# Optimization experiments

Measured on AMD Instinct MI355X. Metric: run time of the kernel, lower is better.

Reference implementation:

```python
import jax, jax.numpy as jnp
import numpy as np

DIM = 512
HEADS = 8
DIM_HEAD = 64  # default dim_head used for scale, matches DIM//HEADS here
SCALE = DIM_HEAD ** -0.5
B, X, Y = 8, 32, 32


def setup_inputs() -> dict:
    key = jax.random.key(0)
    k0, k1, k2, k3 = jax.random.split(key, 4)
    fmap = jax.random.normal(k0, (B, DIM, X, Y), dtype=jnp.float32)
    # 1x1 convs as matrices: weight [out, in]
    Wqkvl = jax.random.normal(k1, (4 * DIM, DIM), dtype=jnp.float32) * (DIM ** -0.5)
    Wout = jax.random.normal(k2, (DIM, DIM), dtype=jnp.float32) * (DIM ** -0.5)
    bout = jax.random.normal(k3, (DIM,), dtype=jnp.float32) * 0.01
    return {"fmap": fmap, "Wqkvl": Wqkvl, "Wout": Wout, "bout": bout}


def reference(fmap, Wqkvl, Wout, bout):
    b, c, x, y = fmap.shape
    h, d = HEADS, c // HEADS
    n = x * y
    # 1x1 conv projection to q,k,v,L
    qkvL = jnp.einsum('oc,bcxy->boxy', Wqkvl, fmap)  # [b, 4c, x, y]
    q, k, v, L = jnp.split(qkvL, 4, axis=1)
    # 'b (h d) x y -> b h (x y) d'
    def to_tokens(t):
        return t.reshape(b, h, d, n).transpose(0, 1, 3, 2)
    q, k, v, L = map(to_tokens, (q, k, v, L))
    dots = jnp.einsum('bhid,bhjd->bhij', q, k) * SCALE  # [b,h,n,n]
    attn = jax.nn.softmax(dots, axis=-1)
    out = jnp.einsum('bhij,bhjd->bhid', attn, v) + L  # [b,h,n,d]
    # 'b h (x y) d -> b (h d) x y'
    out = out.transpose(0, 1, 3, 2).reshape(b, c, x, y)
    # output 1x1 conv with bias (dropout=0 -> identity)
    out = jnp.einsum('oc,bcxy->boxy', Wout, out) + bout[None, :, None, None]
    return out
```

## Files before the change

### kernel.cpp

```cpp
#include <hip/hip_runtime.h>

#define Bn 8
#define Cn 512
#define Hn 8
#define Dn 64
#define Nn 1024
#define SCALEQ 0.18033688011112042f

typedef unsigned short u16;
typedef unsigned short u16x8 __attribute__((ext_vector_type(8)));
typedef unsigned short u16x4 __attribute__((ext_vector_type(4)));
typedef short s16x4 __attribute__((ext_vector_type(4)));
typedef float f32x4 __attribute__((ext_vector_type(4)));
typedef __bf16 bf16x8 __attribute__((ext_vector_type(8)));

__device__ __forceinline__ u16 f2bf(float f){
  unsigned u = __float_as_uint(f);
  u += 0x7fffu + ((u >> 16) & 1u);
  return (u16)(u >> 16);
}
__device__ __forceinline__ float bf2f(u16 h){
  return __uint_as_float(((unsigned)h) << 16);
}
__device__ __forceinline__ f32x4 mfma16(u16x8 a, u16x8 b, f32x4 c){
  return __builtin_amdgcn_mfma_f32_16x16x32_bf16(
      __builtin_bit_cast(bf16x8, a), __builtin_bit_cast(bf16x8, b), c, 0, 0, 0);
}
__device__ __forceinline__ f32x4 mfma16k16(u16x4 a, u16x4 b, f32x4 c){
  return __builtin_amdgcn_mfma_f32_16x16x16bf16_1k(
      __builtin_bit_cast(s16x4, a), __builtin_bit_cast(s16x4, b), c, 0, 0, 0);
}

__device__ __forceinline__ void gload16(const u16* src, u16* dst){
  __builtin_amdgcn_global_load_lds(
      (const __attribute__((address_space(1))) unsigned int*)src,
      (__attribute__((address_space(3))) unsigned int*)dst, 16, 0, 0);
}

__global__ __launch_bounds__(256) void k_convert2(const float* __restrict__ s1,
                                                  const float* __restrict__ s2,
                                                  u16* __restrict__ d1, u16* __restrict__ d2,
                                                  int n1, int n2){
  int i = blockIdx.x * 256 + threadIdx.x;
  const float* s; u16* d; int j;
  if (i < n1){ s = s1; d = d1; j = i; }
  else { if (i >= n1 + n2) return; s = s2; d = d2; j = i - n1; }
  float4 f = reinterpret_cast<const float4*>(s)[j];
  u16x4 o;
  o[0] = f2bf(f.x); o[1] = f2bf(f.y); o[2] = f2bf(f.z); o[3] = f2bf(f.w);
  reinterpret_cast<u16x4*>(d)[j] = o;
}

__global__ __launch_bounds__(256) void k_transpose(const float* __restrict__ fmap,
                                                   u16* __restrict__ fmapT){
  __shared__ float tile[64][33];
  const int n0 = blockIdx.x * 32, c0 = blockIdx.y * 64, b = blockIdx.z;
  const int tx = threadIdx.x & 31, ty = threadIdx.x >> 5;
  const float* src = fmap + ((size_t)b * Cn + c0) * Nn + n0;
#pragma unroll
  for (int i = 0; i < 8; i++) tile[ty + 8*i][tx] = src[(size_t)(ty + 8*i) * Nn + tx];
  __syncthreads();
  const int nr = threadIdx.x >> 3;
  const int cj = (threadIdx.x & 7) * 8;
  u16x8 o;
#pragma unroll
  for (int k = 0; k < 8; k++) o[k] = f2bf(tile[cj + k][nr]);
  *reinterpret_cast<u16x8*>(fmapT + ((size_t)b * Nn + n0 + nr) * Cn + c0 + cj) = o;
}

__device__ __forceinline__ void stage64(const u16* g, size_t ldg, u16* lbase, int w, int lane){
#pragma unroll
  for (int s = 0; s < 2; s++){
    int row = s*32 + w*8 + (lane>>3);
    gload16(g + (size_t)row*ldg + (((lane&7) ^ (row&7)) * 8), lbase + (s*32 + w*8)*64);
  }
}
__device__ __forceinline__ void stage128x32(const u16* g, size_t ldg, u16* lbase, int w, int lane){
#pragma unroll
  for (int s = 0; s < 2; s++){
    int row = s*64 + w*16 + (lane>>2);
    gload16(g + (size_t)row*ldg + (((lane&3) ^ (row&3)) * 8), lbase + (s*64 + w*16)*32);
  }
}
__device__ __forceinline__ void stage64x32(const u16* g, size_t ldg, u16* lbase, int w, int lane){
  int row = w*16 + (lane>>2);
  gload16(g + (size_t)row*ldg + (((lane&3) ^ (row&3)) * 8), lbase + (w*16)*32);
}

__device__ __forceinline__ void gemm_fma(const u16x8 (&af)[4], const u16x8 (&bf)[4],
                                         f32x4 (&acc)[4][4]){
#pragma unroll
  for (int i = 0; i < 4; i++)
#pragma unroll
    for (int j = 0; j < 4; j++)
      acc[i][j] = mfma16(af[i], bf[j], acc[i][j]);
}

__device__ __forceinline__ void gemm_nt_128(const u16* __restrict__ Ap, int lda,
                                            const u16* __restrict__ Bp, int ldb,
                                            u16* sA, u16* sB,
                                            f32x4 (&acc)[4][4]){
  const int tid = threadIdx.x;
  const int w = tid >> 6, lane = tid & 63, r = lane & 15, g = lane >> 4;
  const int wi = w >> 1, wj = w & 1;
  stage128x32(Ap, lda, sA, w, lane);
  stage128x32(Bp, ldb, sB, w, lane);
  for (int ks = 0; ks < Cn/32; ks++){
    __syncthreads();
    const int cur = ks & 1;
    if (ks + 1 < Cn/32){
      stage128x32(Ap + (ks+1)*32, lda, sA + (cur^1)*128*32, w, lane);
      stage128x32(Bp + (ks+1)*32, ldb, sB + (cur^1)*128*32, w, lane);
    }
    const u16* Al = sA + cur*128*32;
    const u16* Bl = sB + cur*128*32;
    u16x8 af[4], bf[4];
#pragma unroll
    for (int t = 0; t < 4; t++){
      int ar = wi*64 + t*16 + r;
      af[t] = *reinterpret_cast<const u16x8*>(&Al[ar*32 + ((g ^ (ar&3)) * 8)]);
      int br = wj*64 + t*16 + r;
      bf[t] = *reinterpret_cast<const u16x8*>(&Bl[br*32 + ((g ^ (br&3)) * 8)]);
    }
    gemm_fma(af, bf, acc);
  }
}

__global__ __launch_bounds__(256) void k_gemm1(const u16* __restrict__ fmapT,
                                               const u16* __restrict__ W1,
                                               u16* __restrict__ Qb, u16* __restrict__ Kb,
                                               u16* __restrict__ Vt, u16* __restrict__ Lb){
  __shared__ u16 sA[2*128*32], sB[2*128*32];
  const int lin = blockIdx.x;
  const int wid = (lin & 7) * 128 + (lin >> 3);
  const int ob = wid & 15, nb = (wid >> 4) & 7, b = wid >> 7;
  const int w = threadIdx.x >> 6, wi = w >> 1, wj = w & 1;
  const int lane = threadIdx.x & 63, r = lane & 15, g = lane >> 4;
  const int seg = ob >> 2;

  f32x4 acc[4][4];
  const f32x4 z = {0.f, 0.f, 0.f, 0.f};
#pragma unroll
  for (int i = 0; i < 4; i++)
#pragma unroll
    for (int j = 0; j < 4; j++) acc[i][j] = z;

  const u16* fbase = fmapT + (size_t)b * Nn * Cn;

  if (seg != 2){
    gemm_nt_128(fbase + (size_t)(nb*128) * Cn, Cn, W1 + (size_t)(ob*128) * Cn, Cn, sA, sB, acc);
    u16* dst = (seg == 0) ? Qb : (seg == 1 ? Kb : Lb);
    const float sc = (seg == 0) ? SCALEQ : 1.0f;
#pragma unroll
    for (int it = 0; it < 4; it++)
#pragma unroll
      for (int jt = 0; jt < 4; jt++)
#pragma unroll
        for (int rr = 0; rr < 4; rr++){
          int n = nb*128 + wi*64 + it*16 + 4*g + rr;
          int o = ob*128 + wj*64 + jt*16 + r;
          dst[((size_t)b * Nn + n) * Cn + (o & 511)] = f2bf(acc[it][jt][rr] * sc);
        }
  } else {
    gemm_nt_128(W1 + (size_t)(ob*128) * Cn, Cn, fbase + (size_t)(nb*128) * Cn, Cn, sA, sB, acc);
#pragma unroll
    for (int it = 0; it < 4; it++)
#pragma unroll
      for (int jt = 0; jt < 4; jt++)
#pragma unroll
        for (int rr = 0; rr < 4; rr++){
          int o = ob*128 + wi*64 + it*16 + 4*g + rr;
          int oo = o - 1024;
          int h = oo >> 6, d = oo & 63;
          int n = nb*128 + wj*64 + jt*16 + r;
          Vt[(((size_t)b * Hn + h) * Dn + d) * Nn + n] = f2bf(acc[it][jt][rr]);
        }
  }
}

__device__ __forceinline__ void attn_tile(const u16* Kc, const u16* Vc,
                                          const u16* kbase, const u16* vbase, int next,
                                          u16* Kn, u16* Vn,
                                          int w, int lane, int r, int g,
                                          u16x8 qA0, u16x8 qA1, u16x8 qB0, u16x8 qB1,
                                          f32x4 (&accA)[4], f32x4 (&accB)[4],
                                          f32x4& accSA, f32x4& accSB){
  const f32x4 z = {0.f, 0.f, 0.f, 0.f};
  __syncthreads();
  if (next < 16){
    stage64(kbase + (size_t)next*64*Cn, Cn, Kn, w, lane);
    stage64(vbase + next*64,            Nn, Vn, w, lane);
  }
  f32x4 sA[4], sB[4];
#pragma unroll
  for (int t = 0; t < 4; t++){
    int row = 16*t + r;
    u16x8 k0 = *reinterpret_cast<const u16x8*>(&Kc[row*64 + ((g     ^ (r&7)) * 8)]);
    u16x8 k1 = *reinterpret_cast<const u16x8*>(&Kc[row*64 + (((4+g) ^ (r&7)) * 8)]);
    sA[t] = mfma16(k0, qA0, z); sA[t] = mfma16(k1, qA1, sA[t]);
    sB[t] = mfma16(k0, qB0, z); sB[t] = mfma16(k1, qB1, sB[t]);
  }
  u16x4 pA[4], pB[4];
#pragma unroll
  for (int t = 0; t < 4; t++)
#pragma unroll
    for (int j = 0; j < 4; j++){
      pA[t][j] = __builtin_bit_cast(u16, (__bf16)exp2f(sA[t][j]));
      pB[t][j] = __builtin_bit_cast(u16, (__bf16)exp2f(sB[t][j]));
    }
  const u16x4 ones = {0x3F80u, 0x3F80u, 0x3F80u, 0x3F80u};
#pragma unroll
  for (int t = 0; t < 4; t++){
    accSA = mfma16k16(ones, pA[t], accSA);
    accSB = mfma16k16(ones, pB[t], accSB);
  }
#pragma unroll
  for (int s = 0; s < 4; s++)
#pragma unroll
    for (int dt = 0; dt < 4; dt++){
      int row = dt*16 + r;
      u16x4 vf = *reinterpret_cast<const u16x4*>(
          &Vc[row*64 + (((2*s + (g>>1)) ^ (r&7)) * 8) + (g&1)*4]);
      accA[dt] = mfma16k16(vf, pA[s], accA[dt]);
      accB[dt] = mfma16k16(vf, pB[s], accB[dt]);
    }
}

__global__ __launch_bounds__(256, 4) void k_attn(const u16* __restrict__ Qb,
                                                 const u16* __restrict__ Kb,
                                                 const u16* __restrict__ Vt,
                                                 const u16* __restrict__ Lb,
                                                 u16* __restrict__ tok){
  __shared__ u16 Kl[2*64*64], Vl[2*64*64];
  const int bid = blockIdx.x;
  const int w0 = (bid & 7) * 64 + (bid >> 3);
  const int qblk = w0 & 7, h = (w0 >> 3) & 7, b = w0 >> 6;
  const int w = threadIdx.x >> 6, lane = threadIdx.x & 63;
  const int r = lane & 15, g = lane >> 4;
  const int qA = qblk * 128 + w * 16;
  const int qB = qA + 64;

  const u16* qrowA = Qb + ((size_t)b * Nn + qA + r) * Cn + h * Dn + 8 * g;
  const u16* qrowB = Qb + ((size_t)b * Nn + qB + r) * Cn + h * Dn + 8 * g;
  u16x8 qA0 = *reinterpret_cast<const u16x8*>(qrowA);
  u16x8 qA1 = *reinterpret_cast<const u16x8*>(qrowA + 32);
  u16x8 qB0 = *reinterpret_cast<const u16x8*>(qrowB);
  u16x8 qB1 = *reinterpret_cast<const u16x8*>(qrowB + 32);

  const u16* kbase = Kb + (size_t)b * Nn * Cn + h * Dn;
  const u16* vbase = Vt + ((size_t)b * Hn + h) * Dn * Nn;

  f32x4 accA[4], accB[4];
  const f32x4 z = {0.f, 0.f, 0.f, 0.f};
#pragma unroll
  for (int dt = 0; dt < 4; dt++){ accA[dt] = z; accB[dt] = z; }
  f32x4 accSA = z, accSB = z;

  u16* Kl0 = Kl, *Kl1 = Kl + 64*64;
  u16* Vl0 = Vl, *Vl1 = Vl + 64*64;
  stage64(kbase, Cn, Kl0, w, lane);
  stage64(vbase, Nn, Vl0, w, lane);

  for (int tile = 0; tile < 16; tile += 2){
    attn_tile(Kl0, Vl0, kbase, vbase, tile + 1, Kl1, Vl1, w, lane, r, g,
              qA0, qA1, qB0, qB1, accA, accB, accSA, accSB);
    attn_tile(Kl1, Vl1, kbase, vbase, tile + 2, Kl0, Vl0, w, lane, r, g,
              qA0, qA1, qB0, qB1, accA, accB, accSA, accSB);
  }

  float linvA = 1.0f / accSA[0];
  float linvB = 1.0f / accSB[0];
#pragma unroll
  for (int half = 0; half < 2; half++){
    const int n = (half ? qB : qA) + r;
    const float linv = half ? linvB : linvA;
    const f32x4* acc = half ? accB : accA;
    const u16* lrow = Lb + ((size_t)b * Nn + n) * Cn + h * Dn;
    u16* trow = tok + ((size_t)b * Nn + n) * Cn + h * Dn;
#pragma unroll
    for (int dt = 0; dt < 4; dt++){
      u16x4 lv = *reinterpret_cast<const u16x4*>(lrow + dt*16 + 4*g);
      u16x4 ov;
#pragma unroll
      for (int rr = 0; rr < 4; rr++)
        ov[rr] = f2bf(acc[dt][rr] * linv + bf2f(lv[rr]));
      *reinterpret_cast<u16x4*>(trow + dt*16 + 4*g) = ov;
    }
  }
}

__global__ __launch_bounds__(256) void k_gemm2(const u16* __restrict__ tok,
                                               const u16* __restrict__ Wo,
                                               const float* __restrict__ bout,
                                               float* __restrict__ out){
  __shared__ u16 sA[2*64*32], sB[2*128*32];
  const int lin = blockIdx.x;
  const int wid = (lin & 7) * 64 + (lin >> 3);
  const int ob = wid & 7, nb = (wid >> 3) & 7, b = wid >> 6;
  const int w = threadIdx.x >> 6, wi = w >> 1, wj = w & 1;
  const int lane = threadIdx.x & 63, r = lane & 15, g = lane >> 4;

  f32x4 acc[2][4];
  const f32x4 z = {0.f, 0.f, 0.f, 0.f};
#pragma unroll
  for (int i = 0; i < 2; i++)
#pragma unroll
    for (int j = 0; j < 4; j++) acc[i][j] = z;

  const u16* Ap = Wo + (size_t)(ob*64) * Cn;
  const u16* Bp = tok + (size_t)b * Nn * Cn + (size_t)(nb*128) * Cn;

  stage64x32(Ap, Cn, sA, w, lane);
  stage128x32(Bp, Cn, sB, w, lane);
  for (int ks = 0; ks < Cn/32; ks++){
    __syncthreads();
    const int cur = ks & 1;
    if (ks + 1 < Cn/32){
      stage64x32(Ap + (ks+1)*32, Cn, sA + (cur^1)*64*32, w, lane);
      stage128x32(Bp + (ks+1)*32, Cn, sB + (cur^1)*128*32, w, lane);
    }
    const u16* Al = sA + cur*64*32;
    const u16* Bl = sB + cur*128*32;
    u16x8 af[2], bf[4];
#pragma unroll
    for (int t = 0; t < 2; t++){
      int ar = wi*32 + t*16 + r;
      af[t] = *reinterpret_cast<const u16x8*>(&Al[ar*32 + ((g ^ (ar&3)) * 8)]);
    }
#pragma unroll
    for (int t = 0; t < 4; t++){
      int br = wj*64 + t*16 + r;
      bf[t] = *reinterpret_cast<const u16x8*>(&Bl[br*32 + ((g ^ (br&3)) * 8)]);
    }
#pragma unroll
    for (int i = 0; i < 2; i++)
#pragma unroll
      for (int j = 0; j < 4; j++)
        acc[i][j] = mfma16(af[i], bf[j], acc[i][j]);
  }

#pragma unroll
  for (int it = 0; it < 2; it++)
#pragma unroll
    for (int jt = 0; jt < 4; jt++)
#pragma unroll
      for (int rr = 0; rr < 4; rr++){
        int o = ob*64 + wi*32 + it*16 + 4*g + rr;
        int n = nb*128 + wj*64 + jt*16 + r;
        out[((size_t)b * Cn + o) * Nn + n] = acc[it][jt][rr] + bout[o];
      }
}

extern "C" void kernel_launch(void* const* d_in, const int* in_sizes, int n_in,
                              void* d_out, int out_size, void* d_ws, size_t ws_size,
                              hipStream_t stream){
  const float* fmap  = (const float*)d_in[0];
  const float* Wqkvl = (const float*)d_in[1];
  const float* Wout  = (const float*)d_in[2];
  const float* bout  = (const float*)d_in[3];
  float* out = (float*)d_out;

  char* ws = (char*)d_ws;
  size_t off = 0;
  auto alloc = [&](size_t bytes) -> void* {
    void* p = ws + off;
    off += (bytes + 255) & ~(size_t)255;
    return p;
  };
  u16* W1bf  = (u16*)alloc((size_t)4*Cn*Cn*2);
  u16* Wobf  = (u16*)alloc((size_t)Cn*Cn*2);
  u16* fmapT = (u16*)alloc((size_t)Bn*Nn*Cn*2);
  u16* Qb    = (u16*)alloc((size_t)Bn*Nn*Cn*2);
  u16* Kb    = (u16*)alloc((size_t)Bn*Nn*Cn*2);
  u16* Lb    = (u16*)alloc((size_t)Bn*Nn*Cn*2);
  u16* Vt    = (u16*)alloc((size_t)Bn*Hn*Dn*Nn*2);
  u16* tok   = fmapT;

  const int n1 = 4*Cn*Cn/4, n2 = Cn*Cn/4;
  hipLaunchKernelGGL(k_convert2, dim3((n1 + n2 + 255)/256), dim3(256), 0, stream,
                     Wqkvl, Wout, W1bf, Wobf, n1, n2);
  hipLaunchKernelGGL(k_transpose, dim3(Nn/32, Cn/64, Bn), dim3(256), 0, stream, fmap, fmapT);
  hipLaunchKernelGGL(k_gemm1, dim3(1024), dim3(256), 0, stream, fmapT, W1bf, Qb, Kb, Vt, Lb);
  hipLaunchKernelGGL(k_attn, dim3(512), dim3(256), 0, stream, Qb, Kb, Vt, Lb, tok);
  hipLaunchKernelGGL(k_gemm2, dim3(512), dim3(256), 0, stream, tok, Wobf, bout, out);
}
```

Before: 93.80 us.

## Triple-buffer LDS staging with partial vmcnt waits and MFMA priority hints

Converts the double-buffered global_load_lds pipelines in the QKV GEMM, attention and output GEMM kernels to three-stage ring buffers with a prefetch distance of two. A single barrier plus an explicit s_waitcnt vmcnt(N) replaces __syncthreads, so one tile's loads can stay in flight while the current tile is computed. MFMA sections are wrapped in s_setprio to favour math-issuing waves. This costs 50% more LDS per block, which could lower occupancy, notably for k_attn with launch_bounds(256,4). The hard-coded vmcnt counts must match the exact number of issued loads.

```diff
diff --git a/kernel.cpp b/kernel.cpp
--- a/kernel.cpp
+++ b/kernel.cpp
@@ -36,6 +36,13 @@
       (const __attribute__((address_space(1))) unsigned int*)src,
       (__attribute__((address_space(3))) unsigned int*)dst, 16, 0, 0);
 }
+
+#define TILE_SYNC(N) do {                                     \
+    asm volatile("s_waitcnt vmcnt(" #N ")" ::: "memory");     \
+    __builtin_amdgcn_sched_barrier(0);                        \
+    __builtin_amdgcn_s_barrier();                             \
+    __builtin_amdgcn_sched_barrier(0);                        \
+  } while(0)
 
 __global__ __launch_bounds__(256) void k_convert2(const float* __restrict__ s1,
                                                   const float* __restrict__ s2,
@@ -87,15 +94,6 @@
   gload16(g + (size_t)row*ldg + (((lane&3) ^ (row&3)) * 8), lbase + (w*16)*32);
 }
 
-__device__ __forceinline__ void gemm_fma(const u16x8 (&af)[4], const u16x8 (&bf)[4],
-                                         f32x4 (&acc)[4][4]){
-#pragma unroll
-  for (int i = 0; i < 4; i++)
-#pragma unroll
-    for (int j = 0; j < 4; j++)
-      acc[i][j] = mfma16(af[i], bf[j], acc[i][j]);
-}
-
 __device__ __forceinline__ void gemm_nt_128(const u16* __restrict__ Ap, int lda,
                                             const u16* __restrict__ Bp, int ldb,
                                             u16* sA, u16* sB,
@@ -103,17 +101,21 @@
   const int tid = threadIdx.x;
   const int w = tid >> 6, lane = tid & 63, r = lane & 15, g = lane >> 4;
   const int wi = w >> 1, wj = w & 1;
-  stage128x32(Ap, lda, sA, w, lane);
-  stage128x32(Bp, ldb, sB, w, lane);
-  for (int ks = 0; ks < Cn/32; ks++){
-    __syncthreads();
-    const int cur = ks & 1;
-    if (ks + 1 < Cn/32){
-      stage128x32(Ap + (ks+1)*32, lda, sA + (cur^1)*128*32, w, lane);
-      stage128x32(Bp + (ks+1)*32, ldb, sB + (cur^1)*128*32, w, lane);
-    }
-    const u16* Al = sA + cur*128*32;
-    const u16* Bl = sB + cur*128*32;
+  stage128x32(Ap,      lda, sA,        w, lane);
+  stage128x32(Bp,      ldb, sB,        w, lane);
+  stage128x32(Ap + 32, lda, sA + 4096, w, lane);
+  stage128x32(Bp + 32, ldb, sB + 4096, w, lane);
+  int cur = 0;
+  for (int ks = 0; ks < 16; ks++){
+    if (ks < 15) TILE_SYNC(4);
+    else         TILE_SYNC(0);
+    if (ks + 2 < 16){
+      int nxt = cur + 2; if (nxt >= 3) nxt -= 3;
+      stage128x32(Ap + (ks+2)*32, lda, sA + nxt*4096, w, lane);
+      stage128x32(Bp + (ks+2)*32, ldb, sB + nxt*4096, w, lane);
+    }
+    const u16* Al = sA + cur*4096;
+    const u16* Bl = sB + cur*4096;
     u16x8 af[4], bf[4];
 #pragma unroll
     for (int t = 0; t < 4; t++){
@@ -122,7 +124,14 @@
       int br = wj*64 + t*16 + r;
       bf[t] = *reinterpret_cast<const u16x8*>(&Bl[br*32 + ((g ^ (br&3)) * 8)]);
     }
-    gemm_fma(af, bf, acc);
+    __builtin_amdgcn_s_setprio(1);
+#pragma unroll
+    for (int i = 0; i < 4; i++)
+#pragma unroll
+      for (int j = 0; j < 4; j++)
+        acc[i][j] = mfma16(af[i], bf[j], acc[i][j]);
+    __builtin_amdgcn_s_setprio(0);
+    cur = (cur == 2) ? 0 : cur + 1;
   }
 }
 
@@ -130,7 +139,7 @@
                                                const u16* __restrict__ W1,
                                                u16* __restrict__ Qb, u16* __restrict__ Kb,
                                                u16* __restrict__ Vt, u16* __restrict__ Lb){
-  __shared__ u16 sA[2*128*32], sB[2*128*32];
+  __shared__ u16 sA[3*128*32], sB[3*128*32];
   const int lin = blockIdx.x;
   const int wid = (lin & 7) * 128 + (lin >> 3);
   const int ob = wid & 15, nb = (wid >> 4) & 7, b = wid >> 7;
@@ -178,60 +187,12 @@
   }
 }
 
-__device__ __forceinline__ void attn_tile(const u16* Kc, const u16* Vc,
-                                          const u16* kbase, const u16* vbase, int next,
-                                          u16* Kn, u16* Vn,
-                                          int w, int lane, int r, int g,
-                                          u16x8 qA0, u16x8 qA1, u16x8 qB0, u16x8 qB1,
-                                          f32x4 (&accA)[4], f32x4 (&accB)[4],
-                                          f32x4& accSA, f32x4& accSB){
-  const f32x4 z = {0.f, 0.f, 0.f, 0.f};
-  __syncthreads();
-  if (next < 16){
-    stage64(kbase + (size_t)next*64*Cn, Cn, Kn, w, lane);
-    stage64(vbase + next*64,            Nn, Vn, w, lane);
-  }
-  f32x4 sA[4], sB[4];
-#pragma unroll
-  for (int t = 0; t < 4; t++){
-    int row = 16*t + r;
-    u16x8 k0 = *reinterpret_cast<const u16x8*>(&Kc[row*64 + ((g     ^ (r&7)) * 8)]);
-    u16x8 k1 = *reinterpret_cast<const u16x8*>(&Kc[row*64 + (((4+g) ^ (r&7)) * 8)]);
-    sA[t] = mfma16(k0, qA0, z); sA[t] = mfma16(k1, qA1, sA[t]);
-    sB[t] = mfma16(k0, qB0, z); sB[t] = mfma16(k1, qB1, sB[t]);
-  }
-  u16x4 pA[4], pB[4];
-#pragma unroll
-  for (int t = 0; t < 4; t++)
-#pragma unroll
-    for (int j = 0; j < 4; j++){
-      pA[t][j] = __builtin_bit_cast(u16, (__bf16)exp2f(sA[t][j]));
-      pB[t][j] = __builtin_bit_cast(u16, (__bf16)exp2f(sB[t][j]));
-    }
-  const u16x4 ones = {0x3F80u, 0x3F80u, 0x3F80u, 0x3F80u};
-#pragma unroll
-  for (int t = 0; t < 4; t++){
-    accSA = mfma16k16(ones, pA[t], accSA);
-    accSB = mfma16k16(ones, pB[t], accSB);
-  }
-#pragma unroll
-  for (int s = 0; s < 4; s++)
-#pragma unroll
-    for (int dt = 0; dt < 4; dt++){
-      int row = dt*16 + r;
-      u16x4 vf = *reinterpret_cast<const u16x4*>(
-          &Vc[row*64 + (((2*s + (g>>1)) ^ (r&7)) * 8) + (g&1)*4]);
-      accA[dt] = mfma16k16(vf, pA[s], accA[dt]);
-      accB[dt] = mfma16k16(vf, pB[s], accB[dt]);
-    }
-}
-
 __global__ __launch_bounds__(256, 4) void k_attn(const u16* __restrict__ Qb,
                                                  const u16* __restrict__ Kb,
                                                  const u16* __restrict__ Vt,
                                                  const u16* __restrict__ Lb,
                                                  u16* __restrict__ tok){
-  __shared__ u16 Kl[2*64*64], Vl[2*64*64];
+  __shared__ u16 Kl[3*64*64], Vl[3*64*64];
   const int bid = blockIdx.x;
   const int w0 = (bid & 7) * 64 + (bid >> 3);
   const int qblk = w0 & 7, h = (w0 >> 3) & 7, b = w0 >> 6;
@@ -256,16 +217,61 @@
   for (int dt = 0; dt < 4; dt++){ accA[dt] = z; accB[dt] = z; }
   f32x4 accSA = z, accSB = z;
 
-  u16* Kl0 = Kl, *Kl1 = Kl + 64*64;
-  u16* Vl0 = Vl, *Vl1 = Vl + 64*64;
-  stage64(kbase, Cn, Kl0, w, lane);
-  stage64(vbase, Nn, Vl0, w, lane);
-
-  for (int tile = 0; tile < 16; tile += 2){
-    attn_tile(Kl0, Vl0, kbase, vbase, tile + 1, Kl1, Vl1, w, lane, r, g,
-              qA0, qA1, qB0, qB1, accA, accB, accSA, accSB);
-    attn_tile(Kl1, Vl1, kbase, vbase, tile + 2, Kl0, Vl0, w, lane, r, g,
-              qA0, qA1, qB0, qB1, accA, accB, accSA, accSB);
+  stage64(kbase,             Cn, Kl,        w, lane);
+  stage64(vbase,             Nn, Vl,        w, lane);
+  stage64(kbase + 64*Cn,     Cn, Kl + 4096, w, lane);
+  stage64(vbase + 64,        Nn, Vl + 4096, w, lane);
+
+  int cur = 0;
+  for (int tile = 0; tile < 16; tile++){
+    if (tile < 15) TILE_SYNC(4);
+    else           TILE_SYNC(0);
+    if (tile + 2 < 16){
+      int nxt = cur + 2; if (nxt >= 3) nxt -= 3;
+      stage64(kbase + (size_t)(tile+2)*64*Cn, Cn, Kl + nxt*4096, w, lane);
+      stage64(vbase + (tile+2)*64,            Nn, Vl + nxt*4096, w, lane);
+    }
+    const u16* Kc = Kl + cur*4096;
+    const u16* Vc = Vl + cur*4096;
+
+    f32x4 sA[4], sB[4];
+    __builtin_amdgcn_s_setprio(1);
+#pragma unroll
+    for (int t = 0; t < 4; t++){
+      int row = 16*t + r;
+      u16x8 k0 = *reinterpret_cast<const u16x8*>(&Kc[row*64 + ((g     ^ (r&7)) * 8)]);
+      u16x8 k1 = *reinterpret_cast<const u16x8*>(&Kc[row*64 + (((4+g) ^ (r&7)) * 8)]);
+      sA[t] = mfma16(k0, qA0, z); sA[t] = mfma16(k1, qA1, sA[t]);
+      sB[t] = mfma16(k0, qB0, z); sB[t] = mfma16(k1, qB1, sB[t]);
+    }
+    __builtin_amdgcn_s_setprio(0);
+    u16x4 pA[4], pB[4];
+#pragma unroll
+    for (int t = 0; t < 4; t++)
+#pragma unroll
+      for (int j = 0; j < 4; j++){
+        pA[t][j] = __builtin_bit_cast(u16, (__bf16)exp2f(sA[t][j]));
+        pB[t][j] = __builtin_bit_cast(u16, (__bf16)exp2f(sB[t][j]));
+      }
+    const u16x4 ones = {0x3F80u, 0x3F80u, 0x3F80u, 0x3F80u};
+    __builtin_amdgcn_s_setprio(1);
+#pragma unroll
+    for (int t = 0; t < 4; t++){
+      accSA = mfma16k16(ones, pA[t], accSA);
+      accSB = mfma16k16(ones, pB[t], accSB);
+    }
+#pragma unroll
+    for (int s = 0; s < 4; s++)
+#pragma unroll
+      for (int dt = 0; dt < 4; dt++){
+        int row = dt*16 + r;
+        u16x4 vf = *reinterpret_cast<const u16x4*>(
+            &Vc[row*64 + (((2*s + (g>>1)) ^ (r&7)) * 8) + (g&1)*4]);
+        accA[dt] = mfma16k16(vf, pA[s], accA[dt]);
+        accB[dt] = mfma16k16(vf, pB[s], accB[dt]);
+      }
+    __builtin_amdgcn_s_setprio(0);
+    cur = (cur == 2) ? 0 : cur + 1;
   }
 
   float linvA = 1.0f / accSA[0];
@@ -293,7 +299,7 @@
                                                const u16* __restrict__ Wo,
                                                const float* __restrict__ bout,
                                                float* __restrict__ out){
-  __shared__ u16 sA[2*64*32], sB[2*128*32];
+  __shared__ u16 sA[3*64*32], sB[3*128*32];
   const int lin = blockIdx.x;
   const int wid = (lin & 7) * 64 + (lin >> 3);
   const int ob = wid & 7, nb = (wid >> 3) & 7, b = wid >> 6;
@@ -310,17 +316,21 @@
   const u16* Ap = Wo + (size_t)(ob*64) * Cn;
   const u16* Bp = tok + (size_t)b * Nn * Cn + (size_t)(nb*128) * Cn;
 
-  stage64x32(Ap, Cn, sA, w, lane);
-  stage128x32(Bp, Cn, sB, w, lane);
-  for (int ks = 0; ks < Cn/32; ks++){
-    __syncthreads();
-    const int cur = ks & 1;
-    if (ks + 1 < Cn/32){
-      stage64x32(Ap + (ks+1)*32, Cn, sA + (cur^1)*64*32, w, lane);
-      stage128x32(Bp + (ks+1)*32, Cn, sB + (cur^1)*128*32, w, lane);
-    }
-    const u16* Al = sA + cur*64*32;
-    const u16* Bl = sB + cur*128*32;
+  stage64x32 (Ap,      Cn, sA,        w, lane);
+  stage128x32(Bp,      Cn, sB,        w, lane);
+  stage64x32 (Ap + 32, Cn, sA + 2048, w, lane);
+  stage128x32(Bp + 32, Cn, sB + 4096, w, lane);
+  int cur = 0;
+  for (int ks = 0; ks < 16; ks++){
+    if (ks < 15) TILE_SYNC(3);
+    else         TILE_SYNC(0);
+    if (ks + 2 < 16){
+      int nxt = cur + 2; if (nxt >= 3) nxt -= 3;
+      stage64x32 (Ap + (ks+2)*32, Cn, sA + nxt*2048, w, lane);
+      stage128x32(Bp + (ks+2)*32, Cn, sB + nxt*4096, w, lane);
+    }
+    const u16* Al = sA + cur*2048;
+    const u16* Bl = sB + cur*4096;
     u16x8 af[2], bf[4];
 #pragma unroll
     for (int t = 0; t < 2; t++){
@@ -332,11 +342,14 @@
       int br = wj*64 + t*16 + r;
       bf[t] = *reinterpret_cast<const u16x8*>(&Bl[br*32 + ((g ^ (br&3)) * 8)]);
     }
+    __builtin_amdgcn_s_setprio(1);
 #pragma unroll
     for (int i = 0; i < 2; i++)
 #pragma unroll
       for (int j = 0; j < 4; j++)
         acc[i][j] = mfma16(af[i], bf[j], acc[i][j]);
+    __builtin_amdgcn_s_setprio(0);
+    cur = (cur == 2) ? 0 : cur + 1;
   }
 
 #pragma unroll
```

Result: no change. 93.00 us (-0.9%).
